# Kernel optimization log

Measured on AMD Instinct MI355X. Metric: run time of the kernel, lower is better.

The kernel has to match this reference:

```python
import jax, jax.numpy as jnp
import numpy as np


def setup_inputs() -> dict:
    key = jax.random.key(0)
    x = jax.random.normal(key, (16, 256, 4096), dtype=jnp.float32)  # (B, C, N)
    return {"x": x}


def reference(x):
    # Original: sigmoid(avgpool_lastdim(x^T @ x)) == sigmoid(x^T @ mean(x, -1))
    # x: (B, C, N). m: (B, C). scores: (B, N).
    m = jnp.mean(x, axis=-1)
    scores = jnp.einsum('bcn,bc->bn', x, m)
    out = jax.nn.sigmoid(scores)
    return out[:, None, None, :]  # (B, 1, 1, N)
```

## Files before the change

### kernel.cpp

```cpp
#include <hip/hip_runtime.h>


#define B_DIM 16
#define C_DIM 256
#define N_DIM 4096
#define CSPLIT 16
#define CCHUNK (C_DIM / CSPLIT)
#define NTILE 1024

__global__ __launch_bounds__(256) void mean_rows_kernel(
    const float* __restrict__ x, float* __restrict__ m) {
  const int row = blockIdx.x;
  const float4* xr = reinterpret_cast<const float4*>(x + (size_t)row * N_DIM);
  float s = 0.0f;
#pragma unroll
  for (int i = 0; i < 4; ++i) {
    float4 v = xr[threadIdx.x + i * 256];
    s += (v.x + v.y) + (v.z + v.w);
  }
#pragma unroll
  for (int off = 32; off > 0; off >>= 1) s += __shfl_down(s, off, 64);
  __shared__ float wsum[4];
  const int lane = threadIdx.x & 63;
  const int wid = threadIdx.x >> 6;
  if (lane == 0) wsum[wid] = s;
  __syncthreads();
  if (threadIdx.x == 0) {
    float t = (wsum[0] + wsum[1]) + (wsum[2] + wsum[3]);
    m[row] = t * (1.0f / (float)N_DIM);
  }
}

__global__ __launch_bounds__(256) void partial_score_kernel(
    const float* __restrict__ x, const float* __restrict__ m,
    float* __restrict__ partials) {
  const int bid = blockIdx.x;
  const int cs = bid & (CSPLIT - 1);
  const int nt = (bid >> 4) & 3;
  const int b = bid >> 6;

  __shared__ float ms[CCHUNK];
  if (threadIdx.x < CCHUNK)
    ms[threadIdx.x] = m[b * C_DIM + cs * CCHUNK + threadIdx.x];
  __syncthreads();

  const int n0 = nt * NTILE + threadIdx.x * 4;
  const float* xb =
      x + (size_t)b * C_DIM * N_DIM + (size_t)(cs * CCHUNK) * N_DIM + n0;

  float4 acc = make_float4(0.f, 0.f, 0.f, 0.f);
#pragma unroll
  for (int c = 0; c < CCHUNK; ++c) {
    float4 v = *reinterpret_cast<const float4*>(xb + (size_t)c * N_DIM);
    float w = ms[c];
    acc.x += v.x * w;
    acc.y += v.y * w;
    acc.z += v.z * w;
    acc.w += v.w * w;
  }
  float* p = partials + ((size_t)cs * B_DIM + b) * N_DIM + n0;
  *reinterpret_cast<float4*>(p) = acc;
}

__global__ __launch_bounds__(256) void reduce_sigmoid_kernel(
    const float* __restrict__ partials, float* __restrict__ out) {
  const int i4 = (blockIdx.x * 256 + threadIdx.x) * 4;
  float4 s = make_float4(0.f, 0.f, 0.f, 0.f);
#pragma unroll
  for (int cs = 0; cs < CSPLIT; ++cs) {
    float4 v = *reinterpret_cast<const float4*>(
        partials + (size_t)cs * (B_DIM * N_DIM) + i4);
    s.x += v.x; s.y += v.y; s.z += v.z; s.w += v.w;
  }
  float4 o;
  o.x = 1.0f / (1.0f + __expf(-s.x));
  o.y = 1.0f / (1.0f + __expf(-s.y));
  o.z = 1.0f / (1.0f + __expf(-s.z));
  o.w = 1.0f / (1.0f + __expf(-s.w));
  *reinterpret_cast<float4*>(out + i4) = o;
}

extern "C" void kernel_launch(void* const* d_in, const int* in_sizes, int n_in,
                              void* d_out, int out_size, void* d_ws,
                              size_t ws_size, hipStream_t stream) {
  const float* x = (const float*)d_in[0];
  float* out = (float*)d_out;
  float* m = (float*)d_ws;
  float* partials = (float*)d_ws + 4096;

  mean_rows_kernel<<<B_DIM * C_DIM, 256, 0, stream>>>(x, m);
  partial_score_kernel<<<B_DIM * (N_DIM / NTILE) * CSPLIT, 256, 0, stream>>>(
      x, m, partials);
  reduce_sigmoid_kernel<<<(B_DIM * N_DIM) / 1024, 256, 0, stream>>>(partials,
                                                                    out);
}
```

Baseline: 99.91 us.

## Fuse mean, partial scores and sigmoid into one cooperative kernel with register-held x

Replaces the three-kernel pipeline with a single cooperative-launch kernel. Each block loads its x tile once into registers, computes partial row sums and atomically accumulates them, then after a grid sync computes weighted partials from the same registers. After a second grid sync, 64 blocks reduce the partials and apply the sigmoid. This removes the second full read of x and two kernel launches. In exchange it adds grid-wide syncs, a memset, atomics, heavy register and LDS use (128 float registers per thread), and host-side occupancy queries on every call.

```diff
diff --git a/kernel.cpp b/kernel.cpp
--- a/kernel.cpp
+++ b/kernel.cpp
@@ -1,12 +1,97 @@
 #include <hip/hip_runtime.h>
+#include <hip/hip_cooperative_groups.h>
 
 
 #define B_DIM 16
 #define C_DIM 256
 #define N_DIM 4096
-#define CSPLIT 16
-#define CCHUNK (C_DIM / CSPLIT)
-#define NTILE 1024
+
+namespace cg = cooperative_groups;
+
+#define CSPLIT 8
+#define CCHUNK 32
+#define COOP_BLKS (B_DIM * CSPLIT * 4)
+
+__global__ __launch_bounds__(256, 2) void fused_kernel(
+    const float* __restrict__ x, float* __restrict__ msum,
+    float* __restrict__ partials, float* __restrict__ out) {
+  cg::grid_group grid = cg::this_grid();
+
+  const int bid = blockIdx.x;
+  const int nt = bid & 3;
+  const int cs = (bid >> 2) & 7;
+  const int b = bid >> 5;
+  const int t = threadIdx.x;
+  const int n0 = nt * 1024 + t * 4;
+
+  __shared__ float lds_sums[256][33];
+  __shared__ float lds2[8][32];
+  __shared__ float lds_m[32];
+
+  const float* xb =
+      x + (size_t)b * C_DIM * N_DIM + (size_t)(cs * CCHUNK) * N_DIM + n0;
+  float4 v[CCHUNK];
+#pragma unroll
+  for (int c = 0; c < CCHUNK; ++c) {
+    v[c] = *reinterpret_cast<const float4*>(xb + (size_t)c * N_DIM);
+    lds_sums[t][c] = (v[c].x + v[c].y) + (v[c].z + v[c].w);
+  }
+  __syncthreads();
+  {
+    const int c = t & 31;
+    const int chunk = t >> 5;
+    float s = 0.0f;
+#pragma unroll
+    for (int r = 0; r < 32; ++r) s += lds_sums[chunk * 32 + r][c];
+    lds2[chunk][c] = s;
+  }
+  __syncthreads();
+  if (t < 32) {
+    float s = 0.0f;
+#pragma unroll
+    for (int ch = 0; ch < 8; ++ch) s += lds2[ch][t];
+    atomicAdd(&msum[b * C_DIM + cs * CCHUNK + t], s);
+  }
+
+  grid.sync();
+
+  if (t < 32) lds_m[t] = msum[b * C_DIM + cs * CCHUNK + t] * (1.0f / N_DIM);
+  __syncthreads();
+  float4 acc = make_float4(0.f, 0.f, 0.f, 0.f);
+#pragma unroll
+  for (int c = 0; c < CCHUNK; ++c) {
+    const float w = lds_m[c];
+    acc.x += v[c].x * w;
+    acc.y += v[c].y * w;
+    acc.z += v[c].z * w;
+    acc.w += v[c].w * w;
+  }
+  *reinterpret_cast<float4*>(partials + ((size_t)cs * B_DIM + b) * N_DIM +
+                             n0) = acc;
+
+  grid.sync();
+
+  if (bid < 64) {
+    const int i4 = (bid * 256 + t) * 4;
+    float4 s = make_float4(0.f, 0.f, 0.f, 0.f);
+#pragma unroll
+    for (int csr = 0; csr < CSPLIT; ++csr) {
+      float4 p = *reinterpret_cast<const float4*>(
+          partials + (size_t)csr * (B_DIM * N_DIM) + i4);
+      s.x += p.x; s.y += p.y; s.z += p.z; s.w += p.w;
+    }
+    float4 o;
+    o.x = 1.0f / (1.0f + __expf(-s.x));
+    o.y = 1.0f / (1.0f + __expf(-s.y));
+    o.z = 1.0f / (1.0f + __expf(-s.z));
+    o.w = 1.0f / (1.0f + __expf(-s.w));
+    *reinterpret_cast<float4*>(out + i4) = o;
+  }
+}
+
+#define FB_CSPLIT 16
+#define FB_CCHUNK 16
+#define FB_NTILE 1024
 
 __global__ __launch_bounds__(256) void mean_rows_kernel(
     const float* __restrict__ x, float* __restrict__ m) {
@@ -35,22 +120,22 @@
     const float* __restrict__ x, const float* __restrict__ m,
     float* __restrict__ partials) {
   const int bid = blockIdx.x;
-  const int cs = bid & (CSPLIT - 1);
+  const int cs = bid & (FB_CSPLIT - 1);
   const int nt = (bid >> 4) & 3;
   const int b = bid >> 6;
 
-  __shared__ float ms[CCHUNK];
-  if (threadIdx.x < CCHUNK)
-    ms[threadIdx.x] = m[b * C_DIM + cs * CCHUNK + threadIdx.x];
-  __syncthreads();
-
-  const int n0 = nt * NTILE + threadIdx.x * 4;
+  __shared__ float ms[FB_CCHUNK];
+  if (threadIdx.x < FB_CCHUNK)
+    ms[threadIdx.x] = m[b * C_DIM + cs * FB_CCHUNK + threadIdx.x];
+  __syncthreads();
+
+  const int n0 = nt * FB_NTILE + threadIdx.x * 4;
   const float* xb =
-      x + (size_t)b * C_DIM * N_DIM + (size_t)(cs * CCHUNK) * N_DIM + n0;
+      x + (size_t)b * C_DIM * N_DIM + (size_t)(cs * FB_CCHUNK) * N_DIM + n0;
 
   float4 acc = make_float4(0.f, 0.f, 0.f, 0.f);
 #pragma unroll
-  for (int c = 0; c < CCHUNK; ++c) {
+  for (int c = 0; c < FB_CCHUNK; ++c) {
     float4 v = *reinterpret_cast<const float4*>(xb + (size_t)c * N_DIM);
     float w = ms[c];
     acc.x += v.x * w;
@@ -67,7 +152,7 @@
   const int i4 = (blockIdx.x * 256 + threadIdx.x) * 4;
   float4 s = make_float4(0.f, 0.f, 0.f, 0.f);
 #pragma unroll
-  for (int cs = 0; cs < CSPLIT; ++cs) {
+  for (int cs = 0; cs < FB_CSPLIT; ++cs) {
     float4 v = *reinterpret_cast<const float4*>(
         partials + (size_t)cs * (B_DIM * N_DIM) + i4);
     s.x += v.x; s.y += v.y; s.z += v.z; s.w += v.w;
@@ -85,12 +170,32 @@
                               size_t ws_size, hipStream_t stream) {
   const float* x = (const float*)d_in[0];
   float* out = (float*)d_out;
-  float* m = (float*)d_ws;
-  float* partials = (float*)d_ws + 4096;
-
-  mean_rows_kernel<<<B_DIM * C_DIM, 256, 0, stream>>>(x, m);
-  partial_score_kernel<<<B_DIM * (N_DIM / NTILE) * CSPLIT, 256, 0, stream>>>(
-      x, m, partials);
+  float* msum = (float*)d_ws;
+  float* partials = (float*)d_ws + B_DIM * C_DIM;
+
+  int coop = 0;
+  (void)hipDeviceGetAttribute(&coop, hipDeviceAttributeCooperativeLaunch, 0);
+  int max_blk_per_cu = 0;
+  (void)hipOccupancyMaxActiveBlocksPerMultiprocessor(
+      &max_blk_per_cu, reinterpret_cast<const void*>(fused_kernel), 256, 0);
+  int num_cu = 0;
+  (void)hipDeviceGetAttribute(&num_cu,
+                              hipDeviceAttributeMultiprocessorCount, 0);
+
+  bool use_coop = (coop != 0) && (max_blk_per_cu * num_cu >= COOP_BLKS);
+
+  if (use_coop) {
+    hipMemsetAsync(msum, 0, B_DIM * C_DIM * sizeof(float), stream);
+    void* args[] = {(void*)&x, (void*)&msum, (void*)&partials, (void*)&out};
+    hipError_t e = hipLaunchCooperativeKernel(
+        reinterpret_cast<void*>(fused_kernel), dim3(COOP_BLKS), dim3(256),
+        args, 0, stream);
+    if (e == hipSuccess) return;
+  }
+
+  mean_rows_kernel<<<B_DIM * C_DIM, 256, 0, stream>>>(x, msum);
+  partial_score_kernel<<<B_DIM * 4 * FB_CSPLIT, 256, 0, stream>>>(x, msum,
+                                                                  partials);
   reduce_sigmoid_kernel<<<(B_DIM * N_DIM) / 1024, 256, 0, stream>>>(partials,
                                                                     out);
 }
```

Result: no change. 99.91 us (+0.0%).
